# Optimization experiments

Measured on AMD Instinct MI355X. Metric: run time of the kernel, lower is better.

The kernel has to match this reference:

```python
import jax, jax.numpy as jnp
import numpy as np

B, N, C = 2, 2048, 1024
H = 8
DH = C // H  # head dim = 128


def setup_inputs() -> dict:
    key = jax.random.key(0)
    ks = jax.random.split(key, 10)
    s = 1.0 / np.sqrt(C)
    return {
        "inputs_q": jax.random.normal(ks[0], (B, N, C), dtype=jnp.float32),
        "inputs_kv": jax.random.normal(ks[1], (B, N, C), dtype=jnp.float32),
        "Wq": jax.random.normal(ks[2], (C, C), dtype=jnp.float32) * s,
        "bq": jnp.zeros((C,), dtype=jnp.float32),
        "Wk": jax.random.normal(ks[3], (C, C), dtype=jnp.float32) * s,
        "bk": jnp.zeros((C,), dtype=jnp.float32),
        "Wv": jax.random.normal(ks[4], (C, C), dtype=jnp.float32) * s,
        "bv": jnp.zeros((C,), dtype=jnp.float32),
        "Wo": jax.random.normal(ks[5], (C, C), dtype=jnp.float32) * s,
        "bo": jnp.zeros((C,), dtype=jnp.float32),
    }


def reference(inputs_q, inputs_kv, Wq, bq, Wk, bk, Wv, bv, Wo, bo):
    # QKV linear projections
    q = inputs_q @ Wq + bq           # [B, N, C]
    k = inputs_kv @ Wk + bk          # [B, M, C]
    v = inputs_kv @ Wv + bv          # [B, M, C]
    # split heads
    q = q.reshape(B, N, H, DH)
    k = k.reshape(B, -1, H, DH)
    v = v.reshape(B, -1, H, DH)
    # explicit attention, matching attend(): scale by 1/sqrt(head_dim)
    attn = jnp.einsum('bnhc,bmhc->bhnm', q, k) * (1.0 / np.sqrt(DH))
    normalized = jax.nn.softmax(attn, axis=-1)  # f32 softmax (inputs are f32)
    summed = jnp.einsum('bhnm,bmhd->bnhd', normalized, v)
    summed = summed.reshape(B, N, C)  # merge heads: ...n(hd)
    # output linear
    return summed @ Wo + bo
```

## Files before the change

kernel.cpp:

```cpp
#include <hip/hip_runtime.h>

typedef unsigned short u16;
typedef __bf16 bf16;
typedef __attribute__((ext_vector_type(8))) __bf16 bf16x8;
typedef __attribute__((ext_vector_type(4))) float f32x4;

#define AS1(p) ((const __attribute__((address_space(1))) void*)(p))
#define AS3(p) ((__attribute__((address_space(3))) void*)(p))

__device__ __forceinline__ u16 f2bf(float f) {
  unsigned u = __builtin_bit_cast(unsigned, f);
  u += 0x7fffu + ((u >> 16) & 1u);
  return (u16)(u >> 16);
}

static constexpr int  B_ = 2, N_ = 2048, C_ = 1024, H_ = 8, DH_ = 128;
static constexpr long SZ_IN = (long)B_ * N_ * C_;
static constexpr long SZ_W  = (long)C_ * C_;

__global__ void k_cast(const float* __restrict__ q, const float* __restrict__ kv,
                       const float* __restrict__ W0, const float* __restrict__ W1,
                       const float* __restrict__ W2, const float* __restrict__ W3,
                       u16* __restrict__ qb, u16* __restrict__ kvb,
                       u16* __restrict__ WT)
{
  __shared__ u16 t[64][65];
  int tid = threadIdx.x;
  if (blockIdx.y < 2) {
    const float* src = blockIdx.y ? kv : q;
    u16* dst = blockIdx.y ? kvb : qb;
    long i = ((long)blockIdx.x * 256 + tid) * 8;
    float4 a = *(const float4*)(src + i);
    float4 b = *(const float4*)(src + i + 4);
    uint4 v;
    v.x = f2bf(a.x) | ((unsigned)f2bf(a.y) << 16);
    v.y = f2bf(a.z) | ((unsigned)f2bf(a.w) << 16);
    v.z = f2bf(b.x) | ((unsigned)f2bf(b.y) << 16);
    v.w = f2bf(b.z) | ((unsigned)f2bf(b.w) << 16);
    *(uint4*)(dst + i) = v;
    return;
  }
  int x = blockIdx.x;
  if (x >= 1024) return;
  int z = x >> 8, tile = x & 255;
  const float* W = (z == 0) ? W0 : (z == 1) ? W1 : (z == 2) ? W2 : W3;
  u16* dst = WT + (long)z * SZ_W;
  int n0 = (tile & 15) * 64, k0 = (tile >> 4) * 64;
#pragma unroll
  for (int r = 0; r < 4; ++r) {
    int slot = r * 256 + tid;
    int row = slot >> 4, c4 = slot & 15;
    float4 a = *(const float4*)(W + (long)(k0 + row) * 1024 + n0 + c4 * 4);
    t[c4*4+0][row] = f2bf(a.x);
    t[c4*4+1][row] = f2bf(a.y);
    t[c4*4+2][row] = f2bf(a.z);
    t[c4*4+3][row] = f2bf(a.w);
  }
  __syncthreads();
#pragma unroll
  for (int r = 0; r < 4; ++r) {
    int slot = r * 256 + tid;
    int row = slot >> 4, c4 = slot & 15;
    uint2 v;
    v.x = t[row][c4*4+0] | ((unsigned)t[row][c4*4+1] << 16);
    v.y = t[row][c4*4+2] | ((unsigned)t[row][c4*4+3] << 16);
    *(uint2*)(dst + (long)(n0 + row) * 1024 + k0 + c4 * 4) = v;
  }
}

__device__ __forceinline__ void gemm_main_128x128(
    const u16* __restrict__ A, const u16* __restrict__ BT,
    u16* lA, u16* lB, int m0, int n0, int tid, f32x4 acc[4][4])
{
  int w = tid >> 6, l = tid & 63, quad = l >> 4, lm = l & 15;
  int wm = w >> 1, wn = w & 1;
  int srow = tid >> 2, schunk = tid & 3;
  int sxw = (srow >> 1) & 3;
  int sxr = (lm >> 1) & 3;
  const u16* Ag = A + (long)(m0 + srow) * 1024 + (schunk ^ sxw) * 8;
  const u16* Bg = BT + (long)(n0 + srow) * 1024 + (schunk ^ sxw) * 8;
  u16* lAw = lA + w * 512;
  u16* lBw = lB + w * 512;
  for (int kb = 0; kb < 32; ++kb) {
    const u16* Agk = Ag + kb * 32;
    const u16* Bgk = Bg + kb * 32;
    __builtin_amdgcn_global_load_lds(AS1(Agk),           AS3(lAw),        16, 0, 0);
    __builtin_amdgcn_global_load_lds(AS1(Agk + 64*1024), AS3(lAw + 2048), 16, 0, 0);
    __builtin_amdgcn_global_load_lds(AS1(Bgk),           AS3(lBw),        16, 0, 0);
    __builtin_amdgcn_global_load_lds(AS1(Bgk + 64*1024), AS3(lBw + 2048), 16, 0, 0);
    __syncthreads();
    bf16x8 af[4], bfr[4];
#pragma unroll
    for (int mi = 0; mi < 4; ++mi)
      af[mi] = *(const bf16x8*)(lA + (wm*64 + mi*16 + lm)*32 + ((quad ^ sxr))*8);
#pragma unroll
    for (int ni = 0; ni < 4; ++ni)
      bfr[ni] = *(const bf16x8*)(lB + (wn*64 + ni*16 + lm)*32 + ((quad ^ sxr))*8);
#pragma unroll
    for (int mi = 0; mi < 4; ++mi)
#pragma unroll
      for (int ni = 0; ni < 4; ++ni)
        acc[mi][ni] = __builtin_amdgcn_mfma_f32_16x16x32_bf16(af[mi], bfr[ni], acc[mi][ni], 0, 0, 0);
    __syncthreads();
  }
}

__global__ __launch_bounds__(256, 3)
void k_gemm_qkv(const u16* __restrict__ qb, const u16* __restrict__ kvb,
                const u16* __restrict__ wt,
                const float* __restrict__ bq, const float* __restrict__ bk,
                const float* __restrict__ bv,
                u16* __restrict__ Qb, u16* __restrict__ Kb, u16* __restrict__ VTb)
{
  __shared__ u16 lA[4096], lB[4096];
  int tid = threadIdx.x;
  int z = blockIdx.z;
  f32x4 acc[4][4] = {};
  int w = tid >> 6, l = tid & 63, quad = l >> 4, lm = l & 15;
  int wm = w >> 1, wn = w & 1;

  if (z == 2) {
    int m0 = blockIdx.y * 128, n0 = blockIdx.x * 128;
    gemm_main_128x128(kvb, wt + 2 * SZ_W, lA, lB, m0, n0, tid, acc);
#pragma unroll
    for (int ni = 0; ni < 4; ++ni) {
      int n = n0 + wn*64 + ni*16 + lm;
      float bb = bv[n];
      int h = n >> 7, dd = n & 127;
#pragma unroll
      for (int mi = 0; mi < 4; ++mi) {
        int mbase = m0 + wm*64 + mi*16 + quad*4;
        int bidx = mbase >> 11, nn = mbase & 2047;
        u16 o0 = f2bf(acc[mi][ni][0] + bb), o1 = f2bf(acc[mi][ni][1] + bb);
        u16 o2 = f2bf(acc[mi][ni][2] + bb), o3 = f2bf(acc[mi][ni][3] + bb);
        uint2 v; v.x = o0 | ((unsigned)o1 << 16); v.y = o2 | ((unsigned)o3 << 16);
        *(uint2*)(VTb + ((long)(bidx*8 + h)*128 + dd)*2048 + nn) = v;
      }
    }
  } else {
    const u16* X = (z == 0) ? qb : kvb;
    const float* bias = (z == 0) ? bq : bk;
    u16* dst = (z == 0) ? Qb : Kb;
    float scale = (z == 0) ? 0.08838834764831845f : 1.0f;
    int m0 = blockIdx.x * 128, n0 = blockIdx.y * 128;
    gemm_main_128x128(wt + (long)z * SZ_W, X, lA, lB, m0, n0, tid, acc);
#pragma unroll
    for (int mi = 0; mi < 4; ++mi) {
      int chb = m0 + wm*64 + mi*16 + quad*4;
      int h = chb >> 7, d = chb & 127;
      float4 bb = *(const float4*)(bias + chb);
#pragma unroll
      for (int ni = 0; ni < 4; ++ni) {
        int tok = n0 + wn*64 + ni*16 + lm;
        int bidx = tok >> 11, nn = tok & 2047;
        u16 o0 = f2bf((acc[mi][ni][0] + bb.x) * scale);
        u16 o1 = f2bf((acc[mi][ni][1] + bb.y) * scale);
        u16 o2 = f2bf((acc[mi][ni][2] + bb.z) * scale);
        u16 o3 = f2bf((acc[mi][ni][3] + bb.w) * scale);
        uint2 v; v.x = o0 | ((unsigned)o1 << 16); v.y = o2 | ((unsigned)o3 << 16);
        *(uint2*)(dst + ((long)(bidx*8 + h)*2048 + nn)*128 + d) = v;
      }
    }
  }
}

__global__ __launch_bounds__(512, 2)
void k_attn(const u16* __restrict__ Qb, const u16* __restrict__ Kb,
            const u16* __restrict__ VTb, u16* __restrict__ Sout)
{
  __shared__ u16 smem[20480];
  u16* lP = smem + 16384;

  int tid = threadIdx.x;
  int w = tid >> 6, l = tid & 63, quad = l >> 4, lm = l & 15;
  int bh = blockIdx.x;
  int q0 = blockIdx.y * 128 + w * 16;
  const u16* Qg = Qb + ((long)bh * 2048 + q0) * 128;
  const u16* Kg = Kb + (long)bh * 2048 * 128;
  const u16* Vg = VTb + (long)bh * 128 * 2048;
  u16* lPw = lP + w * 512;

  bf16x8 qf[4];
#pragma unroll
  for (int kk = 0; kk < 4; ++kk)
    qf[kk] = *(const bf16x8*)(Qg + (long)lm * 128 + kk*32 + quad*8);

  f32x4 accO[8] = {};
  float sumP[4] = {};

  auto stage = [&](int tt) {
    int buf = (tt & 1) * 4096;
    {
      int r = w*4 + (l >> 4);
      int c = l & 15;
      __builtin_amdgcn_global_load_lds(
          AS1(Kg + (long)(tt*32 + r)*128 + ((c ^ (r & 7)) * 8)),
          AS3(smem + buf + w*512), 16, 0, 0);
    }
    {
      int dd = w*8 + (l >> 3);
      int c2 = (l & 7) ^ (l >> 3);
      int d  = dd*2 + (c2 >> 2);
      int c  = c2 & 3;
      __builtin_amdgcn_global_load_lds(
          AS1(Vg + (long)d*2048 + tt*32 + c*8),
          AS3(smem + 8192 + buf + w*512), 16, 0, 0);
    }
  };

  stage(0);

#pragma unroll 1
  for (int t = 0; t < 64; ++t) {
    __syncthreads();
    if (t < 63) stage(t + 1);

    const u16* bK = smem + (t & 1) * 4096;
    const u16* bV = smem + 8192 + (t & 1) * 4096;

    f32x4 accS[2] = {};
#pragma unroll
    for (int kk = 0; kk < 4; ++kk)
#pragma unroll
      for (int ni = 0; ni < 2; ++ni) {
        bf16x8 kf = *(const bf16x8*)(bK + (ni*16 + lm)*128 + (((kk*4 + quad) ^ (lm & 7)))*8);
        accS[ni] = __builtin_amdgcn_mfma_f32_16x16x32_bf16(qf[kk], kf, accS[ni], 0, 0, 0);
      }

    bf16x8 vf[8];
#pragma unroll
    for (int ni = 0; ni < 8; ++ni) {
      int dd = ni*8 + (lm >> 1);
      int slot = (((lm & 1)*4 + quad) ^ (lm >> 1));
      vf[ni] = *(const bf16x8*)(bV + dd*64 + slot*8);
    }

#pragma unroll
    for (int r = 0; r < 4; ++r) {
      int R = quad*4 + r;
      int xr = (R >> 1) & 3;
#pragma unroll
      for (int ni = 0; ni < 2; ++ni) {
        float p = __expf(accS[ni][r]);
        sumP[r] += p;
        int ch = ni*2 + (lm >> 3);
        lPw[(R*4 + (ch ^ xr))*8 + (lm & 7)] = f2bf(p);
      }
    }

    bf16x8 pf = *(const bf16x8*)(lPw + (lm*4 + (quad ^ ((lm >> 1) & 3)))*8);

#pragma unroll
    for (int ni = 0; ni < 8; ++ni)
      accO[ni] = __builtin_amdgcn_mfma_f32_16x16x32_bf16(pf, vf[ni], accO[ni], 0, 0, 0);
  }

  int b = bh >> 3, h = bh & 7;
#pragma unroll
  for (int r = 0; r < 4; ++r) {
    float s = sumP[r];
    s += __shfl_xor(s, 1);
    s += __shfl_xor(s, 2);
    s += __shfl_xor(s, 4);
    s += __shfl_xor(s, 8);
    float linv = 1.f / s;
#pragma unroll
    for (int ni = 0; ni < 8; ++ni) {
      float v = accO[ni][r] * linv;
      Sout[((long)(b*2048 + q0 + quad*4 + r))*1024 + h*128 + ni*16 + lm] = f2bf(v);
    }
  }
}

__global__ __launch_bounds__(256, 3)
void k_gemm_out(const u16* __restrict__ S, const u16* __restrict__ WoT,
                const float* __restrict__ bo, float* __restrict__ out)
{
  __shared__ u16 lA[4096], lB[4096];
  int tid = threadIdx.x;
  int m0 = blockIdx.x * 128, n0 = blockIdx.y * 128;
  f32x4 acc[4][4] = {};
  gemm_main_128x128(WoT, S, lA, lB, m0, n0, tid, acc);

  int w = tid >> 6, l = tid & 63, quad = l >> 4, lm = l & 15;
  int wm = w >> 1, wn = w & 1;
#pragma unroll
  for (int mi = 0; mi < 4; ++mi) {
    int chb = m0 + wm*64 + mi*16 + quad*4;
    float4 bb = *(const float4*)(bo + chb);
#pragma unroll
    for (int ni = 0; ni < 4; ++ni) {
      int tok = n0 + wn*64 + ni*16 + lm;
      float4 v;
      v.x = acc[mi][ni][0] + bb.x;
      v.y = acc[mi][ni][1] + bb.y;
      v.z = acc[mi][ni][2] + bb.z;
      v.w = acc[mi][ni][3] + bb.w;
      *(float4*)(out + (long)tok * 1024 + chb) = v;
    }
  }
}

extern "C" void kernel_launch(void* const* d_in, const int* in_sizes, int n_in,
                              void* d_out, int out_size, void* d_ws, size_t ws_size,
                              hipStream_t stream)
{
  const float* inq  = (const float*)d_in[0];
  const float* inkv = (const float*)d_in[1];
  const float* Wq = (const float*)d_in[2];
  const float* bq = (const float*)d_in[3];
  const float* Wk = (const float*)d_in[4];
  const float* bk = (const float*)d_in[5];
  const float* Wv = (const float*)d_in[6];
  const float* bv = (const float*)d_in[7];
  const float* Wo = (const float*)d_in[8];
  const float* bo = (const float*)d_in[9];

  u16* ws   = (u16*)d_ws;
  u16* ABUF = ws;
  u16* KVB  = ws + SZ_IN;
  u16* WT   = ws + 2 * SZ_IN;
  u16* Qb   = WT + 4 * SZ_W;
  u16* Kb   = Qb + SZ_IN;
  u16* VTb  = Kb + SZ_IN;

  k_cast    <<<dim3(2048, 3),   256, 0, stream>>>(inq, inkv, Wq, Wk, Wv, Wo, ABUF, KVB, WT);
  k_gemm_qkv<<<dim3(8, 32, 3),  256, 0, stream>>>(ABUF, KVB, WT, bq, bk, bv, Qb, Kb, VTb);
  k_attn    <<<dim3(16, 16),    512, 0, stream>>>(Qb, Kb, VTb, ABUF);
  k_gemm_out<<<dim3(8, 32),     256, 0, stream>>>(ABUF, WT + 3 * SZ_W, bo, (float*)d_out);
}
```

Baseline: 219.5 us.

## Give each attention wave two 16-row query tiles to reuse K/V fragments

Halves the attention block to 256 threads (4 waves) and has each wave handle 32 query rows as two 16-row MFMA tiles. K and V fragments read from LDS are reused across both query tiles, which halves LDS reads per MFMA. Each wave now issues two cooperative staging loads per tile. In exchange, register pressure roughly doubles for the accumulators and fewer waves per block are available to hide latency.

```diff
diff --git a/kernel.cpp b/kernel.cpp
--- a/kernel.cpp
+++ b/kernel.cpp
@@ -164,7 +164,7 @@
   }
 }
 
-__global__ __launch_bounds__(512, 2)
+__global__ __launch_bounds__(256, 2)
 void k_attn(const u16* __restrict__ Qb, const u16* __restrict__ Kb,
             const u16* __restrict__ VTb, u16* __restrict__ Sout)
 {
@@ -174,37 +174,42 @@
   int tid = threadIdx.x;
   int w = tid >> 6, l = tid & 63, quad = l >> 4, lm = l & 15;
   int bh = blockIdx.x;
-  int q0 = blockIdx.y * 128 + w * 16;
+  int q0 = blockIdx.y * 128 + w * 32;
   const u16* Qg = Qb + ((long)bh * 2048 + q0) * 128;
   const u16* Kg = Kb + (long)bh * 2048 * 128;
   const u16* Vg = VTb + (long)bh * 128 * 2048;
-  u16* lPw = lP + w * 512;
-
-  bf16x8 qf[4];
-#pragma unroll
-  for (int kk = 0; kk < 4; ++kk)
-    qf[kk] = *(const bf16x8*)(Qg + (long)lm * 128 + kk*32 + quad*8);
-
-  f32x4 accO[8] = {};
-  float sumP[4] = {};
+  u16* lPw = lP + w * 1024;
+
+  bf16x8 qf[2][4];
+#pragma unroll
+  for (int mi = 0; mi < 2; ++mi)
+#pragma unroll
+    for (int kk = 0; kk < 4; ++kk)
+      qf[mi][kk] = *(const bf16x8*)(Qg + (long)(mi*16 + lm)*128 + kk*32 + quad*8);
+
+  f32x4 accO[2][8] = {};
+  float sumP[2][4] = {};
 
   auto stage = [&](int tt) {
     int buf = (tt & 1) * 4096;
-    {
-      int r = w*4 + (l >> 4);
-      int c = l & 15;
+#pragma unroll
+    for (int j = 0; j < 2; ++j) {
+      int s = (w*2 + j)*64 + l;
+      int r = s >> 4, c = s & 15;
       __builtin_amdgcn_global_load_lds(
           AS1(Kg + (long)(tt*32 + r)*128 + ((c ^ (r & 7)) * 8)),
-          AS3(smem + buf + w*512), 16, 0, 0);
-    }
-    {
-      int dd = w*8 + (l >> 3);
-      int c2 = (l & 7) ^ (l >> 3);
+          AS3(smem + buf + (w*2 + j)*512), 16, 0, 0);
+    }
+#pragma unroll
+    for (int j = 0; j < 2; ++j) {
+      int s = (w*2 + j)*64 + l;
+      int dd = s >> 3, slot = s & 7;
+      int c2 = slot ^ (dd & 7);
       int d  = dd*2 + (c2 >> 2);
       int c  = c2 & 3;
       __builtin_amdgcn_global_load_lds(
           AS1(Vg + (long)d*2048 + tt*32 + c*8),
-          AS3(smem + 8192 + buf + w*512), 16, 0, 0);
+          AS3(smem + 8192 + buf + (w*2 + j)*512), 16, 0, 0);
     }
   };
 
@@ -218,13 +223,15 @@
     const u16* bK = smem + (t & 1) * 4096;
     const u16* bV = smem + 8192 + (t & 1) * 4096;
 
-    f32x4 accS[2] = {};
+    f32x4 accS[2][2] = {};
 #pragma unroll
     for (int kk = 0; kk < 4; ++kk)
 #pragma unroll
       for (int ni = 0; ni < 2; ++ni) {
         bf16x8 kf = *(const bf16x8*)(bK + (ni*16 + lm)*128 + (((kk*4 + quad) ^ (lm & 7)))*8);
-        accS[ni] = __builtin_amdgcn_mfma_f32_16x16x32_bf16(qf[kk], kf, accS[ni], 0, 0, 0);
+#pragma unroll
+        for (int mi = 0; mi < 2; ++mi)
+          accS[mi][ni] = __builtin_amdgcn_mfma_f32_16x16x32_bf16(qf[mi][kk], kf, accS[mi][ni], 0, 0, 0);
       }
 
     bf16x8 vf[8];
@@ -236,40 +243,49 @@
     }
 
 #pragma unroll
+    for (int mi = 0; mi < 2; ++mi)
+#pragma unroll
+      for (int r = 0; r < 4; ++r) {
+        int R = mi*16 + quad*4 + r;
+        int xr = (quad*2 + (r >> 1)) & 3;
+#pragma unroll
+        for (int ni = 0; ni < 2; ++ni) {
+          float p = __expf(accS[mi][ni][r]);
+          sumP[mi][r] += p;
+          int ch = ni*2 + (lm >> 3);
+          lPw[(R*4 + (ch ^ xr))*8 + (lm & 7)] = f2bf(p);
+        }
+      }
+
+    bf16x8 pf[2];
+#pragma unroll
+    for (int mi = 0; mi < 2; ++mi)
+      pf[mi] = *(const bf16x8*)(lPw + ((mi*16 + lm)*4 + (quad ^ ((lm >> 1) & 3)))*8);
+
+#pragma unroll
+    for (int ni = 0; ni < 8; ++ni)
+#pragma unroll
+      for (int mi = 0; mi < 2; ++mi)
+        accO[mi][ni] = __builtin_amdgcn_mfma_f32_16x16x32_bf16(pf[mi], vf[ni], accO[mi][ni], 0, 0, 0);
+  }
+
+  int b = bh >> 3, h = bh & 7;
+#pragma unroll
+  for (int mi = 0; mi < 2; ++mi)
+#pragma unroll
     for (int r = 0; r < 4; ++r) {
-      int R = quad*4 + r;
-      int xr = (R >> 1) & 3;
-#pragma unroll
-      for (int ni = 0; ni < 2; ++ni) {
-        float p = __expf(accS[ni][r]);
-        sumP[r] += p;
-        int ch = ni*2 + (lm >> 3);
-        lPw[(R*4 + (ch ^ xr))*8 + (lm & 7)] = f2bf(p);
-      }
-    }
-
-    bf16x8 pf = *(const bf16x8*)(lPw + (lm*4 + (quad ^ ((lm >> 1) & 3)))*8);
-
-#pragma unroll
-    for (int ni = 0; ni < 8; ++ni)
-      accO[ni] = __builtin_amdgcn_mfma_f32_16x16x32_bf16(pf, vf[ni], accO[ni], 0, 0, 0);
-  }
-
-  int b = bh >> 3, h = bh & 7;
-#pragma unroll
-  for (int r = 0; r < 4; ++r) {
-    float s = sumP[r];
-    s += __shfl_xor(s, 1);
-    s += __shfl_xor(s, 2);
-    s += __shfl_xor(s, 4);
-    s += __shfl_xor(s, 8);
-    float linv = 1.f / s;
-#pragma unroll
-    for (int ni = 0; ni < 8; ++ni) {
-      float v = accO[ni][r] * linv;
-      Sout[((long)(b*2048 + q0 + quad*4 + r))*1024 + h*128 + ni*16 + lm] = f2bf(v);
-    }
-  }
+      float s = sumP[mi][r];
+      s += __shfl_xor(s, 1);
+      s += __shfl_xor(s, 2);
+      s += __shfl_xor(s, 4);
+      s += __shfl_xor(s, 8);
+      float linv = 1.f / s;
+#pragma unroll
+      for (int ni = 0; ni < 8; ++ni) {
+        float v = accO[mi][ni][r] * linv;
+        Sout[((long)(b*2048 + q0 + mi*16 + quad*4 + r))*1024 + h*128 + ni*16 + lm] = f2bf(v);
+      }
+    }
 }
 
 __global__ __launch_bounds__(256, 3)
@@ -326,6 +342,6 @@
 
   k_cast    <<<dim3(2048, 3),   256, 0, stream>>>(inq, inkv, Wq, Wk, Wv, Wo, ABUF, KVB, WT);
   k_gemm_qkv<<<dim3(8, 32, 3),  256, 0, stream>>>(ABUF, KVB, WT, bq, bk, bv, Qb, Kb, VTb);
-  k_attn    <<<dim3(16, 16),    512, 0, stream>>>(Qb, Kb, VTb, ABUF);
+  k_attn    <<<dim3(16, 16),    256, 0, stream>>>(Qb, Kb, VTb, ABUF);
   k_gemm_out<<<dim3(8, 32),     256, 0, stream>>>(ABUF, WT + 3 * SZ_W, bo, (float*)d_out);
 }
```

After: 226.2 us. 1.03x slower.
